# Optimization experiments

Measured on AMD Instinct MI355X. Metric: run time of the kernel, lower is better.

The kernel has to match this reference:

```python
import jax, jax.numpy as jnp
import numpy as np

# ---- module constants (from init_kwargs) ----
W, H = 320, 240
VOXEL_SIZE = 0.05
DEPTH_MIN = 0.1 / VOXEL_SIZE          # 2.0  (voxel units, as in the torch module)
DEPTH_MAX = 4.0 / VOXEL_SIZE          # 80.0
STEP = 0.5                            # ray_increment = voxel_size/2 -> half a voxel in grid units
N_STEPS = int((DEPTH_MAX - DEPTH_MIN) / STEP)   # 156 ray-march steps
IGNORE = -1                           # config.data.ignore_label
DX, DY, DZ = 192, 192, 96             # dims3d (x, y, z); occ3d stored [B, Dz, Dy, Dx]
N_VOX, C_FEAT = 80000, 128
B, V = 1, 2


def setup_inputs() -> dict:
    key = jax.random.key(0)
    k1, k2, k3, k4 = jax.random.split(key, 4)
    features_3d = jax.random.normal(k1, (N_VOX, C_FEAT), dtype=jnp.float32)
    # occupied-voxel coordinates scattered into dense index grid (SparseTensor.dense())
    xi = jax.random.randint(k2, (N_VOX,), 0, DX)
    yi = jax.random.randint(k3, (N_VOX,), 0, DY)
    zi = jax.random.randint(k4, (N_VOX,), 0, DZ)
    occ3d = jnp.full((B, DZ, DY, DX), IGNORE, dtype=jnp.int32)
    occ3d = occ3d.at[0, zi, yi, xi].set(jnp.arange(N_VOX, dtype=jnp.int32))
    # camera-to-grid poses: identity rotation, camera inside grid looking +z
    vm = jnp.tile(jnp.eye(4, dtype=jnp.float32)[None, None], (B, V, 1, 1))
    trans = jnp.array([[96.0, 96.0, 2.0], [80.0, 100.0, 3.0]], dtype=jnp.float32)
    vm = vm.at[:, :, :3, 3].set(trans[None])
    intr = jnp.tile(jnp.array([280.0, 280.0, 160.0, 120.0], dtype=jnp.float32)[None, None], (B, V, 1))
    return {"features_3d": features_3d, "view_matrix": vm,
            "intrinsic_params": intr, "occ3d": occ3d}


_CORNERS = [(dz, dy, dx) for dz in (0, 1) for dy in (0, 1) for dx in (0, 1)]


def _corner_lookup(occ3d, base, bb):
    """Gather the 8 corner voxel indices around base [..., 3] = (x, y, z)."""
    Dz, Dy, Dx = occ3d.shape[1:]
    idxs, valids = [], []
    for dz, dy, dx in _CORNERS:
        cx = base[..., 0] + dx
        cy = base[..., 1] + dy
        cz = base[..., 2] + dz
        inb = (cx >= 0) & (cx < Dx) & (cy >= 0) & (cy < Dy) & (cz >= 0) & (cz < Dz)
        idx = occ3d[bb, jnp.clip(cz, 0, Dz - 1), jnp.clip(cy, 0, Dy - 1), jnp.clip(cx, 0, Dx - 1)]
        idxs.append(idx)
        valids.append(inb & (idx != IGNORE))
    return idxs, valids


def reference(features_3d, view_matrix, intrinsic_params, occ3d):
    Bv, Vv = view_matrix.shape[:2]
    N, C = features_3d.shape
    fx = intrinsic_params[..., 0][..., None, None]   # [B,V,1,1]
    fy = intrinsic_params[..., 1][..., None, None]
    cx = intrinsic_params[..., 2][..., None, None]
    cy = intrinsic_params[..., 3][..., None, None]
    u = jnp.arange(W, dtype=jnp.float32) + 0.5
    v = jnp.arange(H, dtype=jnp.float32) + 0.5
    uu, vv = jnp.meshgrid(u, v)                      # [H,W]
    dirs_cam = jnp.stack([(uu[None, None] - cx) / fx,
                          (vv[None, None] - cy) / fy,
                          jnp.broadcast_to(jnp.float32(1.0), (Bv, Vv, H, W))], axis=-1)  # [B,V,H,W,3]
    R = view_matrix[..., :3, :3]
    t = view_matrix[..., :3, 3]
    dirs = jnp.einsum('bvij,bvhwj->bvhwi', R, dirs_cam)   # ray dirs in grid space
    origin = t[:, :, None, None, :]
    bb = jnp.arange(Bv)[:, None, None, None]               # batch index, broadcasts

    hit0 = jnp.zeros((Bv, Vv, H, W), dtype=bool)
    base0 = jnp.zeros((Bv, Vv, H, W, 3), dtype=jnp.int32)
    frac0 = jnp.zeros((Bv, Vv, H, W, 3), dtype=jnp.float32)
    depths = DEPTH_MIN + STEP * jnp.arange(N_STEPS, dtype=jnp.float32)

    def step(carry, d):
        hit, base, frac = carry
        p = origin + d * dirs - 0.5                        # corner-interp frame
        b0 = jnp.floor(p).astype(jnp.int32)
        fr = (p - b0).astype(jnp.float32)
        _, valids = _corner_lookup(occ3d, b0, bb)
        occ_any = valids[0]
        for vd in valids[1:]:
            occ_any = occ_any | vd
        new = occ_any & (~hit)                             # first-hit semantics
        base = jnp.where(new[..., None], b0, base)
        frac = jnp.where(new[..., None], fr, frac)
        return (hit | occ_any, base, frac), None

    (hit, base, frac), _ = jax.lax.scan(step, (hit0, base0, frac0), depths)

    idxs, valids = _corner_lookup(occ3d, base, bb)
    hitf = hit.astype(jnp.float32)
    fxw, fyw, fzw = frac[..., 0], frac[..., 1], frac[..., 2]
    ws = []
    for k, (dz, dy, dx) in enumerate(_CORNERS):
        w = ((fzw if dz else 1.0 - fzw) *
             (fyw if dy else 1.0 - fyw) *
             (fxw if dx else 1.0 - fxw))
        ws.append(w * valids[k].astype(jnp.float32) * hitf)
    wsum = ws[0]
    for w in ws[1:]:
        wsum = wsum + w
    inv = 1.0 / (wsum + 1e-8)

    projected = jnp.zeros((Bv, Vv, H, W, C), dtype=jnp.float32)
    norm_ws, masked_idx = [], []
    for k in range(8):
        w = ws[k] * inv
        norm_ws.append(w)
        projected = projected + w[..., None] * features_3d[jnp.clip(idxs[k], 0, N - 1)]
        masked_idx.append(jnp.where(valids[k] & hit, idxs[k], IGNORE))

    indexes_image = jnp.stack(masked_idx, axis=-1)         # [B,V,H,W,8]
    vox_dist_weights = jnp.stack(norm_ws, axis=-1)         # [B,V,H,W,8]

    flat_idx = indexes_image.reshape(-1)
    contrib = (flat_idx != IGNORE).astype(jnp.float32)
    mapping3dto2d_num = jax.ops.segment_sum(contrib, jnp.clip(flat_idx, 0, N - 1), num_segments=N)

    return projected, indexes_image, vox_dist_weights, mapping3dto2d_num
```

## Files before the change

kernel.cpp:

```cpp
#include <hip/hip_runtime.h>
#include <limits.h>

#define W_IMG 320
#define H_IMG 240
#define N_VIEW 2
#define DX_ 192
#define DY_ 192
#define DZ_ 96
#define NVOX 80000
#define CFEAT 128
#define NSTEPS 156
#define NPIX (N_VIEW * H_IMG * W_IMG)

#define NCELLS (DZ_ * DY_ * DX_)
#define WPR (DX_ / 32)
#define NWORDS (NCELLS / 32)

#define OFF_PROJ 0
#define OFF_IDX  (NPIX * CFEAT)
#define OFF_W    (OFF_IDX + NPIX * 8)
#define OFF_MAP  (OFF_W + NPIX * 8)

#define WS_COPIES_OFF 884736

__global__ __launch_bounds__(256) void bitmask_kernel(
    const int* __restrict__ occ, unsigned* __restrict__ bm,
    float* __restrict__ zero_tgt, int zero_n4)
{
    int t = blockIdx.x * 256 + threadIdx.x;
    if (t < zero_n4) ((float4*)zero_tgt)[t] = make_float4(0.f, 0.f, 0.f, 0.f);
    bool occu = (occ[t] != -1);
    unsigned long long b = __ballot(occu);
    if ((threadIdx.x & 63) == 0) {
        int w = t >> 5;
        bm[w]     = (unsigned)b;
        bm[w + 1] = (unsigned)(b >> 32);
    }
}

__global__ __launch_bounds__(256) void dilate_kernel(
    const unsigned* __restrict__ bm, unsigned* __restrict__ dil)
{
    int w = blockIdx.x * 256 + threadIdx.x;
    if (w >= NWORDS) return;
    int wx = w % WPR;
    int y  = (w / WPR) % DY_;
    int z  = w / (WPR * DY_);
    unsigned acc = 0;
    #pragma unroll
    for (int dz = 0; dz < 2; ++dz) {
        #pragma unroll
        for (int dy = 0; dy < 2; ++dy) {
            int zz = z + dz, yy = y + dy;
            if (zz < DZ_ && yy < DY_) {
                int rb = (zz * DY_ + yy) * WPR + wx;
                unsigned m   = bm[rb];
                unsigned nxt = (wx + 1 < WPR) ? bm[rb + 1] : 0u;
                acc |= m | (m >> 1) | ((nxt & 1u) << 31);
            }
        }
    }
    dil[w] = acc;
}

__device__ __forceinline__ bool slow_any(const int* __restrict__ occ,
                                         int ix, int iy, int iz)
{
    bool any = false;
    #pragma unroll
    for (int c = 0; c < 8; ++c) {
        int ddz = c >> 2, ddy = (c >> 1) & 1, ddx = c & 1;
        int cxl = ix + ddx, cyl = iy + ddy, czl = iz + ddz;
        bool inb = ((unsigned)cxl < DX_) & ((unsigned)cyl < DY_) & ((unsigned)czl < DZ_);
        int xc = min(max(cxl, 0), DX_ - 1);
        int yc = min(max(cyl, 0), DY_ - 1);
        int zc = min(max(czl, 0), DZ_ - 1);
        int idx = occ[(zc * DY_ + yc) * DX_ + xc];
        any = any | (inb & (idx != -1));
    }
    return any;
}

__global__ __launch_bounds__(256) void raycast_kernel(
    const float* __restrict__ vm,
    const float* __restrict__ intr,
    const int*   __restrict__ occ,
    const unsigned* __restrict__ dil,
    float* __restrict__ out_idx,
    float* __restrict__ out_w,
    float* __restrict__ map_base,
    int copy_mask)
{
    int t    = blockIdx.x * 256 + threadIdx.x;
    int pix  = t >> 2;
    int sub  = t & 3;
    int lane = threadIdx.x & 63;

    int v   = pix / (H_IMG * W_IMG);
    int rem = pix - v * (H_IMG * W_IMG);
    int h   = rem / W_IMG;
    int w   = rem - h * W_IMG;

    const float* M = vm + v * 16;
    const float* I = intr + v * 4;
    float fx = I[0], fy = I[1], cx = I[2], cy = I[3];
    float uu = (float)w + 0.5f;
    float vv = (float)h + 0.5f;
    float dc0 = __fdiv_rn(__fsub_rn(uu, cx), fx);
    float dc1 = __fdiv_rn(__fsub_rn(vv, cy), fy);
    float dc2 = 1.0f;
    float dir0 = __fadd_rn(__fadd_rn(__fmul_rn(M[0], dc0), __fmul_rn(M[1], dc1)), __fmul_rn(M[2], dc2));
    float dir1 = __fadd_rn(__fadd_rn(__fmul_rn(M[4], dc0), __fmul_rn(M[5], dc1)), __fmul_rn(M[6], dc2));
    float dir2 = __fadd_rn(__fadd_rn(__fmul_rn(M[8], dc0), __fmul_rn(M[9], dc1)), __fmul_rn(M[10], dc2));
    float t0 = M[3], t1 = M[7], t2 = M[11];

    int s_hit = INT_MAX;
    for (int base = 0; base < NSTEPS; base += 16) {
        int smin = INT_MAX;
        #pragma unroll
        for (int j = 0; j < 4; ++j) {
            int s = base + sub + 4 * j;
            bool any = false;
            if (s < NSTEPS) {
                float d  = __fadd_rn(2.0f, __fmul_rn(0.5f, (float)s));
                float px = __fsub_rn(__fadd_rn(t0, __fmul_rn(d, dir0)), 0.5f);
                float py = __fsub_rn(__fadd_rn(t1, __fmul_rn(d, dir1)), 0.5f);
                float pz = __fsub_rn(__fadd_rn(t2, __fmul_rn(d, dir2)), 0.5f);
                int ix = (int)floorf(px);
                int iy = (int)floorf(py);
                int iz = (int)floorf(pz);
                if (((unsigned)ix < DX_) & ((unsigned)iy < DY_) & ((unsigned)iz < DZ_)) {
                    unsigned wd = dil[(iz * DY_ + iy) * WPR + (ix >> 5)];
                    any = (wd >> (ix & 31)) & 1u;
                } else if (ix >= -1 && ix < DX_ && iy >= -1 && iy < DY_ && iz >= -1 && iz < DZ_) {
                    any = slow_any(occ, ix, iy, iz);
                }
            }
            if (any) smin = min(smin, s);
        }
        smin = min(smin, __shfl_xor(smin, 1));
        smin = min(smin, __shfl_xor(smin, 2));
        if (smin != INT_MAX) { s_hit = smin; break; }
    }

    int hit = 0;
    int bx = 0, by = 0, bz = 0;
    float fr0 = 0.f, fr1 = 0.f, fr2 = 0.f;
    if (s_hit != INT_MAX) {
        hit = 1;
        float d  = __fadd_rn(2.0f, __fmul_rn(0.5f, (float)s_hit));
        float px = __fsub_rn(__fadd_rn(t0, __fmul_rn(d, dir0)), 0.5f);
        float py = __fsub_rn(__fadd_rn(t1, __fmul_rn(d, dir1)), 0.5f);
        float pz = __fsub_rn(__fadd_rn(t2, __fmul_rn(d, dir2)), 0.5f);
        float fpx = floorf(px), fpy = floorf(py), fpz = floorf(pz);
        bx = (int)fpx; by = (int)fpy; bz = (int)fpz;
        fr0 = px - fpx; fr1 = py - fpy; fr2 = pz - fpz;
    }

    float ws8[8];
    int   id8[8];
    float wsum = 0.0f;
    #pragma unroll
    for (int c = 0; c < 8; ++c) {
        float wk = 0.0f;
        int idv = -1;
        if (hit) {
            int ddz = c >> 2, ddy = (c >> 1) & 1, ddx = c & 1;
            int cxl = bx + ddx, cyl = by + ddy, czl = bz + ddz;
            bool inb = ((unsigned)cxl < DX_) & ((unsigned)cyl < DY_) & ((unsigned)czl < DZ_);
            int xc = min(max(cxl, 0), DX_ - 1);
            int yc = min(max(cyl, 0), DY_ - 1);
            int zc = min(max(czl, 0), DZ_ - 1);
            int idx = occ[(zc * DY_ + yc) * DX_ + xc];
            bool valid = inb & (idx != -1);
            float gw = ddz ? fr2 : (1.0f - fr2);
            gw = __fmul_rn(gw, ddy ? fr1 : (1.0f - fr1));
            gw = __fmul_rn(gw, ddx ? fr0 : (1.0f - fr0));
            if (valid) { wk = gw; idv = idx; }
        }
        ws8[c] = wk;
        id8[c] = idv;
        wsum = __fadd_rn(wsum, wk);
    }
    float inv = __fdiv_rn(1.0f, __fadd_rn(wsum, 1e-8f));

    float wn[8];
    #pragma unroll
    for (int c = 0; c < 8; ++c) wn[c] = __fmul_rn(ws8[c], inv);

    float4* w4 = (float4*)out_w;
    float4* i4 = (float4*)out_idx;
    if (sub == 0)      w4[pix * 2]     = make_float4(wn[0], wn[1], wn[2], wn[3]);
    else if (sub == 1) w4[pix * 2 + 1] = make_float4(wn[4], wn[5], wn[6], wn[7]);
    else if (sub == 2) i4[pix * 2]     = make_float4((float)id8[0], (float)id8[1], (float)id8[2], (float)id8[3]);
    else               i4[pix * 2 + 1] = make_float4((float)id8[4], (float)id8[5], (float)id8[6], (float)id8[7]);

    float* mymap = map_base + (int)(blockIdx.x & copy_mask) * NVOX;
    #pragma unroll
    for (int c = 0; c < 8; ++c) {
        int vid  = id8[c];
        int prev = __shfl(vid, max(lane - 4, 0));
        bool leader = (lane < 4) || (vid != prev);
        unsigned long long lm = __ballot(leader);
        int gl = lane & ~3;
        unsigned long long higher = (gl == 60) ? 0ULL : (lm >> (gl + 4));
        int cnt = higher ? (((__ffsll(higher) - 1) >> 2) + 1) : ((64 - gl) >> 2);
        if (sub == 0 && leader && vid >= 0) atomicAdd(&mymap[vid], (float)cnt);
    }
}

__global__ __launch_bounds__(256) void reduce_map_kernel(
    const float* __restrict__ copies, float* __restrict__ out_map, int nc)
{
    int t = blockIdx.x * 256 + threadIdx.x;
    if (t >= NVOX / 4) return;
    const float4* c4 = (const float4*)copies;
    float4 s = c4[t];
    for (int c = 1; c < nc; ++c) {
        float4 a = c4[c * (NVOX / 4) + t];
        s.x += a.x; s.y += a.y; s.z += a.z; s.w += a.w;
    }
    ((float4*)out_map)[t] = s;
}

__global__ __launch_bounds__(256) void gather_kernel(
    const float* __restrict__ feat,
    const float* __restrict__ out_idx,
    const float* __restrict__ out_w,
    float* __restrict__ proj)
{
    int t = blockIdx.x * 256 + threadIdx.x;
    int pix  = t >> 5;
    int lane = t & 31;
    if (pix >= NPIX) return;

    const float4* f4 = (const float4*)feat;
    float4 acc = make_float4(0.f, 0.f, 0.f, 0.f);
    #pragma unroll
    for (int c = 0; c < 8; ++c) {
        float wk = out_w[pix * 8 + c];
        if (wk != 0.0f) {
            int idx = (int)out_idx[pix * 8 + c];
            float4 f = f4[idx * (CFEAT / 4) + lane];
            acc.x += wk * f.x;
            acc.y += wk * f.y;
            acc.z += wk * f.z;
            acc.w += wk * f.w;
        }
    }
    ((float4*)proj)[pix * (CFEAT / 4) + lane] = acc;
}

extern "C" void kernel_launch(void* const* d_in, const int* in_sizes, int n_in,
                              void* d_out, int out_size, void* d_ws, size_t ws_size,
                              hipStream_t stream) {
    const float* feat = (const float*)d_in[0];
    const float* vm   = (const float*)d_in[1];
    const float* intr = (const float*)d_in[2];
    const int*   occ  = (const int*)d_in[3];
    float* out = (float*)d_out;

    float* out_proj = out + OFF_PROJ;
    float* out_idx  = out + OFF_IDX;
    float* out_w    = out + OFF_W;
    float* out_map  = out + OFF_MAP;

    unsigned* bm  = (unsigned*)d_ws;
    unsigned* dil = bm + NWORDS;
    float* copies = (float*)((char*)d_ws + WS_COPIES_OFF);

    size_t avail = ws_size > WS_COPIES_OFF ? ws_size - WS_COPIES_OFF : 0;
    int nc = (int)(avail / (NVOX * sizeof(float)));
    nc = nc >= 8 ? 8 : (nc >= 4 ? 4 : (nc >= 2 ? 2 : (nc >= 1 ? 1 : 0)));

    float* map_base = nc ? copies : out_map;
    int copy_mask   = nc ? nc - 1 : 0;
    float* zero_tgt = nc ? copies : out_map;
    int zero_n4     = (nc ? nc : 1) * (NVOX / 4);

    bitmask_kernel<<<NCELLS / 256, 256, 0, stream>>>(occ, bm, zero_tgt, zero_n4);
    dilate_kernel<<<(NWORDS + 255) / 256, 256, 0, stream>>>(bm, dil);

    raycast_kernel<<<(NPIX * 4) / 256, 256, 0, stream>>>(
        vm, intr, occ, dil, out_idx, out_w, map_base, copy_mask);

    if (nc)
        reduce_map_kernel<<<(NVOX / 4 + 255) / 256, 256, 0, stream>>>(
            copies, out_map, nc);

    gather_kernel<<<(NPIX * 32) / 256, 256, 0, stream>>>(
        feat, out_idx, out_w, out_proj);
}
```

Before: 65.06 us.

## Fuse bitmask into dilation, batch raycast probes, merge map reduce into gather

Builds the dilated occupancy bitmask straight from the occupancy grid in one kernel, dropping the separate bitmask pass and its intermediate buffer. The raycast loop now tests 32 steps per iteration with branchless dilated-mask loads and defers boundary slow-path checks to a rare second pass. The map-copy reduction is folded into the gather launch as extra blocks. Together these cut two kernel launches and raise memory-level parallelism in the ray march. The cost is that each dilation word re-reads up to four occupancy rows, and the ray march may evaluate steps past the first hit.

```diff
diff --git a/kernel.cpp b/kernel.cpp
--- a/kernel.cpp
+++ b/kernel.cpp
@@ -21,43 +21,46 @@
 #define OFF_W    (OFF_IDX + NPIX * 8)
 #define OFF_MAP  (OFF_W + NPIX * 8)
 
-#define WS_COPIES_OFF 884736
-
-__global__ __launch_bounds__(256) void bitmask_kernel(
-    const int* __restrict__ occ, unsigned* __restrict__ bm,
+#define WS_COPIES_OFF 442368
+
+#define GATHER_BLOCKS (NPIX * 32 / 256)
+
+__global__ __launch_bounds__(256) void dilate_direct_kernel(
+    const int* __restrict__ occ, unsigned* __restrict__ dil,
     float* __restrict__ zero_tgt, int zero_n4)
 {
-    int t = blockIdx.x * 256 + threadIdx.x;
-    if (t < zero_n4) ((float4*)zero_tgt)[t] = make_float4(0.f, 0.f, 0.f, 0.f);
-    bool occu = (occ[t] != -1);
-    unsigned long long b = __ballot(occu);
-    if ((threadIdx.x & 63) == 0) {
-        int w = t >> 5;
-        bm[w]     = (unsigned)b;
-        bm[w + 1] = (unsigned)(b >> 32);
-    }
-}
-
-__global__ __launch_bounds__(256) void dilate_kernel(
-    const unsigned* __restrict__ bm, unsigned* __restrict__ dil)
-{
     int w = blockIdx.x * 256 + threadIdx.x;
+    int zt = w * 2;
+    if (zt < zero_n4)     ((float4*)zero_tgt)[zt]     = make_float4(0.f, 0.f, 0.f, 0.f);
+    if (zt + 1 < zero_n4) ((float4*)zero_tgt)[zt + 1] = make_float4(0.f, 0.f, 0.f, 0.f);
     if (w >= NWORDS) return;
+
     int wx = w % WPR;
     int y  = (w / WPR) % DY_;
     int z  = w / (WPR * DY_);
     unsigned acc = 0;
     #pragma unroll
     for (int dz = 0; dz < 2; ++dz) {
+        int zz = z + dz;
+        if (zz >= DZ_) continue;
         #pragma unroll
         for (int dy = 0; dy < 2; ++dy) {
-            int zz = z + dz, yy = y + dy;
-            if (zz < DZ_ && yy < DY_) {
-                int rb = (zz * DY_ + yy) * WPR + wx;
-                unsigned m   = bm[rb];
-                unsigned nxt = (wx + 1 < WPR) ? bm[rb + 1] : 0u;
-                acc |= m | (m >> 1) | ((nxt & 1u) << 31);
+            int yy = y + dy;
+            if (yy >= DY_) continue;
+            const int* row = occ + (zz * DY_ + yy) * DX_ + (wx << 5);
+            const int4* r4 = (const int4*)row;
+            unsigned m = 0;
+            #pragma unroll
+            for (int k = 0; k < 8; ++k) {
+                int4 q = r4[k];
+                unsigned b = (unsigned)(q.x != -1)
+                           | ((unsigned)(q.y != -1) << 1)
+                           | ((unsigned)(q.z != -1) << 2)
+                           | ((unsigned)(q.w != -1) << 3);
+                m |= b << (k * 4);
             }
+            unsigned nxt = (wx + 1 < WPR) ? (unsigned)(row[32] != -1) : 0u;
+            acc |= m | (m >> 1) | (nxt << 31);
         }
     }
     dil[w] = acc;
@@ -115,28 +118,43 @@
     float t0 = M[3], t1 = M[7], t2 = M[11];
 
     int s_hit = INT_MAX;
-    for (int base = 0; base < NSTEPS; base += 16) {
+    for (int base = 0; base < NSTEPS; base += 32) {
         int smin = INT_MAX;
+        int need = 0;
         #pragma unroll
-        for (int j = 0; j < 4; ++j) {
+        for (int j = 0; j < 8; ++j) {
             int s = base + sub + 4 * j;
-            bool any = false;
-            if (s < NSTEPS) {
-                float d  = __fadd_rn(2.0f, __fmul_rn(0.5f, (float)s));
-                float px = __fsub_rn(__fadd_rn(t0, __fmul_rn(d, dir0)), 0.5f);
-                float py = __fsub_rn(__fadd_rn(t1, __fmul_rn(d, dir1)), 0.5f);
-                float pz = __fsub_rn(__fadd_rn(t2, __fmul_rn(d, dir2)), 0.5f);
-                int ix = (int)floorf(px);
-                int iy = (int)floorf(py);
-                int iz = (int)floorf(pz);
-                if (((unsigned)ix < DX_) & ((unsigned)iy < DY_) & ((unsigned)iz < DZ_)) {
-                    unsigned wd = dil[(iz * DY_ + iy) * WPR + (ix >> 5)];
-                    any = (wd >> (ix & 31)) & 1u;
-                } else if (ix >= -1 && ix < DX_ && iy >= -1 && iy < DY_ && iz >= -1 && iz < DZ_) {
-                    any = slow_any(occ, ix, iy, iz);
+            float d  = __fadd_rn(2.0f, __fmul_rn(0.5f, (float)s));
+            float px = __fsub_rn(__fadd_rn(t0, __fmul_rn(d, dir0)), 0.5f);
+            float py = __fsub_rn(__fadd_rn(t1, __fmul_rn(d, dir1)), 0.5f);
+            float pz = __fsub_rn(__fadd_rn(t2, __fmul_rn(d, dir2)), 0.5f);
+            int ix = (int)floorf(px);
+            int iy = (int)floorf(py);
+            int iz = (int)floorf(pz);
+            bool inb3 = ((unsigned)ix < DX_) & ((unsigned)iy < DY_) & ((unsigned)iz < DZ_);
+            int addr = inb3 ? ((iz * DY_ + iy) * WPR + (ix >> 5)) : 0;
+            unsigned wd = dil[addr];
+            bool ok = (s < NSTEPS);
+            bool any = ok & inb3 & (bool)((wd >> (ix & 31)) & 1u);
+            bool ns  = ok & !inb3 & (ix >= -1) & (ix < DX_) & (iy >= -1) & (iy < DY_)
+                          & (iz >= -1) & (iz < DZ_);
+            need |= (ns ? 1 : 0) << j;
+            if (any) smin = min(smin, s);
+        }
+        if (__builtin_expect(need, 0)) {
+            for (int j = 0; j < 8; ++j) {
+                if ((need >> j) & 1) {
+                    int s = base + sub + 4 * j;
+                    float d  = __fadd_rn(2.0f, __fmul_rn(0.5f, (float)s));
+                    float px = __fsub_rn(__fadd_rn(t0, __fmul_rn(d, dir0)), 0.5f);
+                    float py = __fsub_rn(__fadd_rn(t1, __fmul_rn(d, dir1)), 0.5f);
+                    float pz = __fsub_rn(__fadd_rn(t2, __fmul_rn(d, dir2)), 0.5f);
+                    int ix = (int)floorf(px);
+                    int iy = (int)floorf(py);
+                    int iz = (int)floorf(pz);
+                    if (slow_any(occ, ix, iy, iz)) smin = min(smin, s);
                 }
             }
-            if (any) smin = min(smin, s);
         }
         smin = min(smin, __shfl_xor(smin, 1));
         smin = min(smin, __shfl_xor(smin, 2));
@@ -209,30 +227,33 @@
     }
 }
 
-__global__ __launch_bounds__(256) void reduce_map_kernel(
-    const float* __restrict__ copies, float* __restrict__ out_map, int nc)
-{
-    int t = blockIdx.x * 256 + threadIdx.x;
-    if (t >= NVOX / 4) return;
-    const float4* c4 = (const float4*)copies;
-    float4 s = c4[t];
-    for (int c = 1; c < nc; ++c) {
-        float4 a = c4[c * (NVOX / 4) + t];
-        s.x += a.x; s.y += a.y; s.z += a.z; s.w += a.w;
-    }
-    ((float4*)out_map)[t] = s;
-}
-
-__global__ __launch_bounds__(256) void gather_kernel(
+__global__ __launch_bounds__(256) void gather_reduce_kernel(
     const float* __restrict__ feat,
     const float* __restrict__ out_idx,
     const float* __restrict__ out_w,
-    float* __restrict__ proj)
+    float* __restrict__ proj,
+    const float* __restrict__ copies,
+    float* __restrict__ out_map,
+    int nc)
 {
+    if (blockIdx.x >= GATHER_BLOCKS) {
+        if (nc > 0) {
+            int t = (blockIdx.x - GATHER_BLOCKS) * 256 + threadIdx.x;
+            if (t < NVOX / 4) {
+                const float4* c4 = (const float4*)copies;
+                float4 s = c4[t];
+                for (int c = 1; c < nc; ++c) {
+                    float4 a = c4[c * (NVOX / 4) + t];
+                    s.x += a.x; s.y += a.y; s.z += a.z; s.w += a.w;
+                }
+                ((float4*)out_map)[t] = s;
+            }
+        }
+        return;
+    }
     int t = blockIdx.x * 256 + threadIdx.x;
     int pix  = t >> 5;
     int lane = t & 31;
-    if (pix >= NPIX) return;
 
     const float4* f4 = (const float4*)feat;
     float4 acc = make_float4(0.f, 0.f, 0.f, 0.f);
@@ -265,8 +286,7 @@
     float* out_w    = out + OFF_W;
     float* out_map  = out + OFF_MAP;
 
-    unsigned* bm  = (unsigned*)d_ws;
-    unsigned* dil = bm + NWORDS;
+    unsigned* dil = (unsigned*)d_ws;
     float* copies = (float*)((char*)d_ws + WS_COPIES_OFF);
 
     size_t avail = ws_size > WS_COPIES_OFF ? ws_size - WS_COPIES_OFF : 0;
@@ -278,16 +298,13 @@
     float* zero_tgt = nc ? copies : out_map;
     int zero_n4     = (nc ? nc : 1) * (NVOX / 4);
 
-    bitmask_kernel<<<NCELLS / 256, 256, 0, stream>>>(occ, bm, zero_tgt, zero_n4);
-    dilate_kernel<<<(NWORDS + 255) / 256, 256, 0, stream>>>(bm, dil);
+    dilate_direct_kernel<<<(NWORDS + 255) / 256, 256, 0, stream>>>(
+        occ, dil, zero_tgt, zero_n4);
 
     raycast_kernel<<<(NPIX * 4) / 256, 256, 0, stream>>>(
         vm, intr, occ, dil, out_idx, out_w, map_base, copy_mask);
 
-    if (nc)
-        reduce_map_kernel<<<(NVOX / 4 + 255) / 256, 256, 0, stream>>>(
-            copies, out_map, nc);
-
-    gather_kernel<<<(NPIX * 32) / 256, 256, 0, stream>>>(
-        feat, out_idx, out_w, out_proj);
-}
+    int reduce_blocks = (NVOX / 4 + 255) / 256;
+    gather_reduce_kernel<<<GATHER_BLOCKS + reduce_blocks, 256, 0, stream>>>(
+        feat, out_idx, out_w, out_proj, copies, out_map, nc);
+}
```

Result: faster. 59.62 us (-8.4%).
